# Optimization experiments

Hardware: AMD Instinct MI355X
Metric: run time of the kernel (lower is better)

Reference implementation:

```python
import jax, jax.numpy as jnp
import numpy as np
import math

EMB_DIM = 1024
NUM_HEADS = 16
D_H = EMB_DIM // NUM_HEADS
B, S = 2, 2048


def setup_inputs() -> dict:
    key = jax.random.key(0)
    ks = jax.random.split(key, 6)
    limit = math.sqrt(6.0 / (EMB_DIM + D_H))  # xavier_uniform per head
    x = jax.random.normal(ks[0], (B, S, EMB_DIM), dtype=jnp.float32)
    Wq = jax.random.uniform(ks[1], (NUM_HEADS, EMB_DIM, D_H), jnp.float32, -limit, limit)
    Wk = jax.random.uniform(ks[2], (NUM_HEADS, EMB_DIM, D_H), jnp.float32, -limit, limit)
    Wv = jax.random.uniform(ks[3], (NUM_HEADS, EMB_DIM, D_H), jnp.float32, -limit, limit)
    bq = jnp.zeros((NUM_HEADS, D_H), jnp.float32)
    bk = jnp.zeros((NUM_HEADS, D_H), jnp.float32)
    bv = jnp.zeros((NUM_HEADS, D_H), jnp.float32)
    limo = math.sqrt(6.0 / (EMB_DIM + EMB_DIM))
    W_O = jax.random.uniform(ks[4], (EMB_DIM, EMB_DIM), jnp.float32, -limo, limo)
    causal_mask = jnp.tril(jnp.ones((S, S), jnp.float32))
    padding_mask = jnp.zeros((B, S), jnp.bool_)  # all-False: nothing padded
    return {"x": x, "Wq": Wq, "bq": bq, "Wk": Wk, "bk": bk, "Wv": Wv,
            "bv": bv, "W_O": W_O, "causal_mask": causal_mask,
            "padding_mask": padding_mask}


def reference(x, Wq, bq, Wk, bk, Wv, bv, W_O, causal_mask, padding_mask):
    # Per-head projections, vectorized over heads: [B,S,E] x [H,E,D] -> [B,H,S,D]
    Q = jnp.einsum('bse,hed->bhsd', x, Wq) + bq[None, :, None, :]
    K = jnp.einsum('bse,hed->bhsd', x, Wk) + bk[None, :, None, :]
    V = jnp.einsum('bse,hed->bhsd', x, Wv) + bv[None, :, None, :]
    scores = jnp.einsum('bhsd,bhtd->bhst', Q, K) / math.sqrt(D_H)
    neg_inf = jnp.float32(-jnp.inf)
    scores = jnp.where(causal_mask[None, None, :, :] == 0, neg_inf, scores)
    scores = jnp.where(padding_mask[:, None, None, :], neg_inf, scores)
    attn = jax.nn.softmax(scores, axis=-1)
    out = jnp.einsum('bhst,bhtd->bhsd', attn, V)  # [B,H,S,D]
    # concat heads in order (dim=-1) -> [B,S,H*D]
    x_concat = out.transpose(0, 2, 1, 3).reshape(B, S, EMB_DIM)
    return x_concat @ W_O
```

## Files before the change

### kernel.cpp

```cpp
#include <hip/hip_runtime.h>
#include <hip/hip_bf16.h>


typedef __hip_bfloat16 bf16;
typedef __attribute__((ext_vector_type(8))) short bfrag;
typedef __attribute__((ext_vector_type(4))) float f32x4;
typedef __attribute__((ext_vector_type(16))) float f32x16;
typedef __attribute__((ext_vector_type(4))) short short4v;

#define MFMA16(a, b, c) __builtin_amdgcn_mfma_f32_16x16x32_bf16(a, b, c, 0, 0, 0)
#define MFMA32(a, b, c) __builtin_amdgcn_mfma_f32_32x32x16_bf16(a, b, c, 0, 0, 0)

__device__ __forceinline__ unsigned pkbf(float a, float b) {
  union { bf16 h[2]; unsigned u; } w;
  w.h[0] = __float2bfloat16(a);
  w.h[1] = __float2bfloat16(b);
  return w.u;
}

__global__ __launch_bounds__(256) void prep_all(const float* __restrict__ x,
                                                const float* __restrict__ Wq,
                                                const float* __restrict__ Wk,
                                                const float* __restrict__ Wv,
                                                const float* __restrict__ Wo,
                                                bf16* __restrict__ xb,
                                                bf16* __restrict__ WqkvT,
                                                bf16* __restrict__ WoT) {
  __shared__ bf16 tile[64][80];
  int id = blockIdx.x;
  int t = threadIdx.x;
  if (id < 2048) {
    int i = id * 2048 + t * 8;
    float4 a = *(const float4*)(x + i);
    float4 b = *(const float4*)(x + i + 4);
    union { bf16 h[8]; bfrag v; } tmp;
    tmp.h[0] = __float2bfloat16(a.x); tmp.h[1] = __float2bfloat16(a.y);
    tmp.h[2] = __float2bfloat16(a.z); tmp.h[3] = __float2bfloat16(a.w);
    tmp.h[4] = __float2bfloat16(b.x); tmp.h[5] = __float2bfloat16(b.y);
    tmp.h[6] = __float2bfloat16(b.z); tmp.h[7] = __float2bfloat16(b.w);
    *(bfrag*)(xb + i) = tmp.v;
    return;
  }
  int wid = id - 2048;
  const float* src;
  bf16* dst;
  int srcld, dstld, r0, c0;
  if (wid < 768) {
    int w = wid >> 8, h = (wid >> 4) & 15;
    r0 = (wid & 15) * 64; c0 = 0;
    src = ((w == 0) ? Wq : (w == 1) ? Wk : Wv) + (long)h * 1024 * 64;
    dst = WqkvT + ((long)w * 1024 + h * 64) * 1024;
    srcld = 64; dstld = 1024;
  } else {
    int j = wid - 768;
    c0 = (j & 15) * 64; r0 = (j >> 4) * 64;
    src = Wo; dst = WoT;
    srcld = 1024; dstld = 1024;
  }
  int lr = t >> 3, lc = (t & 7) << 3;
#pragma unroll
  for (int p = 0; p < 2; ++p) {
    int r = lr + p * 32;
    const float* s = src + (long)(r0 + r) * srcld + c0 + lc;
    union { bf16 h8[8]; bfrag v; } tmp;
#pragma unroll
    for (int j = 0; j < 8; ++j) tmp.h8[j] = __float2bfloat16(s[j]);
    *(bfrag*)(&tile[r][lc]) = tmp.v;
  }
  __syncthreads();
#pragma unroll
  for (int p = 0; p < 2; ++p) {
    int c = lr + p * 32;
    union { bf16 h8[8]; bfrag v; } tmp;
#pragma unroll
    for (int j = 0; j < 8; ++j) tmp.h8[j] = tile[lc + j][c];
    *(bfrag*)(dst + (long)(c0 + c) * dstld + r0 + lc) = tmp.v;
  }
}

__global__ __launch_bounds__(256) void gemm_qkv128(const bf16* __restrict__ xb,
                                                   const bf16* __restrict__ WT,
                                                   const float* __restrict__ bq,
                                                   const float* __restrict__ bk,
                                                   const float* __restrict__ bv,
                                                   bf16* __restrict__ Q,
                                                   bf16* __restrict__ K_,
                                                   bf16* __restrict__ Vt) {
  const int K = 1024;
  __shared__ bf16 As[128][72];
  __shared__ bf16 Bs[128][72];
  int id = blockIdx.x;
  int xcd = id & 7, sw = id >> 3;
  int m0 = ((xcd << 2) | (sw & 3)) * 128;
  int n0 = (sw >> 2) * 128;
  int t = threadIdx.x, wave = t >> 6, lane = t & 63, quad = lane >> 4, col = lane & 15;
  int wr = (wave >> 1) * 64, wc = (wave & 1) * 64;
  f32x4 acc[4][4] = {};

  int srow = t >> 1, scol = (t & 1) * 32;
  const bf16* Ag = xb + (long)(m0 + srow) * K + scol;
  const bf16* Bg = WT + (long)(n0 + srow) * K + scol;

  bfrag A0[4], B0[4], A1[4], B1[4];
#pragma unroll
  for (int i = 0; i < 4; ++i) {
    A0[i] = *(const bfrag*)(Ag + 8 * i);
    B0[i] = *(const bfrag*)(Bg + 8 * i);
    A1[i] = *(const bfrag*)(Ag + 64 + 8 * i);
    B1[i] = *(const bfrag*)(Bg + 64 + 8 * i);
  }

  for (int k0 = 0; k0 < K; k0 += 64) {
    __syncthreads();
#pragma unroll
    for (int i = 0; i < 4; ++i) {
      *(bfrag*)(&As[srow][scol + 8 * i]) = A0[i];
      *(bfrag*)(&Bs[srow][scol + 8 * i]) = B0[i];
    }
    int kn = (k0 + 128 < K) ? k0 + 128 : K - 64;
#pragma unroll
    for (int i = 0; i < 4; ++i) {
      A0[i] = A1[i]; B0[i] = B1[i];
      A1[i] = *(const bfrag*)(Ag + kn + 8 * i);
      B1[i] = *(const bfrag*)(Bg + kn + 8 * i);
    }
    __syncthreads();
#pragma unroll
    for (int kc = 0; kc < 2; ++kc) {
      bfrag ra[4], rb[4];
#pragma unroll
      for (int i = 0; i < 4; ++i)
        ra[i] = *(const bfrag*)(&As[wr + 16 * i + col][kc * 32 + quad * 8]);
#pragma unroll
      for (int c = 0; c < 4; ++c)
        rb[c] = *(const bfrag*)(&Bs[wc + 16 * c + col][kc * 32 + quad * 8]);
#pragma unroll
      for (int c = 0; c < 4; ++c)
#pragma unroll
        for (int i = 0; i < 4; ++i) acc[c][i] = MFMA16(ra[i], rb[c], acc[c][i]);
    }
  }

  int sel = n0 >> 10;
  const float* bias = (sel == 0) ? bq : (sel == 1) ? bk : bv;
#pragma unroll
  for (int c = 0; c < 4; ++c) {
    int nn = (n0 + wc + 16 * c + col) & 1023;
    float bvv = bias[nn];
    int h = nn >> 6, d = nn & 63;
#pragma unroll
    for (int i = 0; i < 4; ++i) {
      int mb = m0 + wr + 16 * i + quad * 4;
      int b = mb >> 11, s0 = mb & 2047;
      if (sel < 2) {
        bf16* dst = (sel == 0) ? Q : K_;
        long base = ((long)((b << 4) + h) * 2048 + s0) * 64 + d;
#pragma unroll
        for (int r = 0; r < 4; ++r)
          dst[base + (long)r * 64] = __float2bfloat16(acc[c][i][r] + bvv);
      } else {
        union { bf16 h4[4]; short4v v; } pk;
#pragma unroll
        for (int r = 0; r < 4; ++r) pk.h4[r] = __float2bfloat16(acc[c][i][r] + bvv);
        *(short4v*)(Vt + (long)(((b << 4) + h) * 64 + d) * 2048 + s0) = pk.v;
      }
    }
  }
}

__global__ __launch_bounds__(256) void gemm_out(const bf16* __restrict__ O,
                                                const bf16* __restrict__ Bt,
                                                float* __restrict__ Cf) {
  const int K = 1024;
  __shared__ bf16 As[128][72];
  __shared__ bf16 Bs[64][72];
  int id = blockIdx.x;
  int xcd = id & 7, sw = id >> 3;
  int m0 = ((xcd << 2) | (sw & 3)) * 128;
  int n0 = (sw >> 2) * 64;
  int t = threadIdx.x;
  int wave = t >> 6, lane = t & 63, quad = lane >> 4, col = lane & 15;
  int wr = (wave >> 1) * 64, wc = (wave & 1) * 32;
  f32x4 acc[2][4] = {};

  int srA = t >> 1, scA = (t & 1) * 32;
  int srB = t >> 2, scB = (t & 3) * 16;
  int mrow = m0 + srA;
  int ob = mrow >> 11, os = mrow & 2047;
  const bf16* Ag = O + (long)ob * 2097152 + (long)os * 64 + scA;
  const bf16* Bg = Bt + (long)(n0 + srB) * K + scB;

  bfrag A0[4], A1[4];
  bfrag B0[2], B1[2];
#pragma unroll
  for (int i = 0; i < 4; ++i) {
    A0[i] = *(const bfrag*)(Ag + 8 * i);
    A1[i] = *(const bfrag*)(Ag + (long)64 * 2048 + 8 * i);
  }
#pragma unroll
  for (int i = 0; i < 2; ++i) {
    B0[i] = *(const bfrag*)(Bg + 8 * i);
    B1[i] = *(const bfrag*)(Bg + 64 + 8 * i);
  }

  for (int k0 = 0; k0 < K; k0 += 64) {
    __syncthreads();
#pragma unroll
    for (int i = 0; i < 4; ++i) *(bfrag*)(&As[srA][scA + 8 * i]) = A0[i];
#pragma unroll
    for (int i = 0; i < 2; ++i) *(bfrag*)(&Bs[srB][scB + 8 * i]) = B0[i];
    int kn = (k0 + 128 < K) ? k0 + 128 : K - 64;
#pragma unroll
    for (int i = 0; i < 4; ++i) {
      A0[i] = A1[i];
      A1[i] = *(const bfrag*)(Ag + (long)kn * 2048 + 8 * i);
    }
#pragma unroll
    for (int i = 0; i < 2; ++i) {
      B0[i] = B1[i];
      B1[i] = *(const bfrag*)(Bg + kn + 8 * i);
    }
    __syncthreads();
#pragma unroll
    for (int kc = 0; kc < 2; ++kc) {
      bfrag ra[4], rb[2];
#pragma unroll
      for (int i = 0; i < 4; ++i)
        ra[i] = *(const bfrag*)(&As[wr + 16 * i + col][kc * 32 + quad * 8]);
#pragma unroll
      for (int c = 0; c < 2; ++c)
        rb[c] = *(const bfrag*)(&Bs[wc + 16 * c + col][kc * 32 + quad * 8]);
#pragma unroll
      for (int c = 0; c < 2; ++c)
#pragma unroll
        for (int i = 0; i < 4; ++i) acc[c][i] = MFMA16(ra[i], rb[c], acc[c][i]);
    }
  }

#pragma unroll
  for (int c = 0; c < 2; ++c) {
    int n = n0 + wc + 16 * c + col;
#pragma unroll
    for (int i = 0; i < 4; ++i)
#pragma unroll
      for (int r = 0; r < 4; ++r) {
        int m = m0 + wr + 16 * i + quad * 4 + r;
        Cf[(long)m * 1024 + n] = acc[c][i][r];
      }
  }
}

__global__ __launch_bounds__(256) void attn_kernel(const bf16* __restrict__ Q,
                                                   const bf16* __restrict__ K_,
                                                   const bf16* __restrict__ Vt,
                                                   bf16* __restrict__ O) {
  int id = blockIdx.x;
  int xcd = id & 7, jj = id >> 3;
  int qt = 31 - (jj >> 2);
  int bh = ((jj & 3) << 3) | xcd;

  __shared__ bf16 Ks[128][72];
  __shared__ bf16 Vs[64][136];

  int t = threadIdx.x, wave = t >> 6, lane = t & 63;
  int qh = wave >> 1, jh = wave & 1, hi = lane >> 5, l5 = lane & 31;

  const float SC2 = 0.18033688f;

  int krow = t >> 3, kg = (t & 7) * 8;
  int vrow = t >> 4, vg = (t & 15) * 8;
  const bf16* Kbase = K_ + ((long)bh * 2048 + krow) * 64 + kg;
  const bf16* Vbase = Vt + ((long)bh * 64 + vrow) * 2048 + vg;

  int q0 = qt * 64;
  int nj = (qt >> 1) + 1;
  int qi = q0 + 32 * qh + l5;

  bfrag qa[4];
  const bf16* qp = Q + ((long)bh * 2048 + q0 + 32 * qh + l5) * 64 + hi * 8;
#pragma unroll
  for (int kd = 0; kd < 4; ++kd) qa[kd] = *(const bfrag*)(qp + kd * 16);

  f32x16 o0, o1;
  float lsum = 0.f;
#pragma unroll
  for (int r = 0; r < 16; ++r) { o0[r] = 0.f; o1[r] = 0.f; }

  bfrag kreg[4], vreg[4];
#pragma unroll
  for (int i = 0; i < 4; ++i)
    kreg[i] = *(const bfrag*)(Kbase + (long)(32 * i) * 64);

  for (int jt = 0; jt < nj; ++jt) {
    int j0 = jt * 128;
    __syncthreads();
#pragma unroll
    for (int i = 0; i < 4; ++i)
      *(bfrag*)(&Ks[krow + 32 * i][kg]) = kreg[i];
    int jn = (jt + 1 < nj) ? (jt + 1) * 128 : jt * 128;
#pragma unroll
    for (int i = 0; i < 4; ++i)
      vreg[i] = *(const bfrag*)(Vbase + (long)(16 * i) * 2048 + j0);
#pragma unroll
    for (int i = 0; i < 4; ++i)
      kreg[i] = *(const bfrag*)(Kbase + (long)(jn + 32 * i) * 64);
    __syncthreads();

    f32x16 s0, s1;
#pragma unroll
    for (int r = 0; r < 16; ++r) { s0[r] = 0.f; s1[r] = 0.f; }
#pragma unroll
    for (int kd = 0; kd < 4; ++kd) {
      bfrag ka0 = *(const bfrag*)(&Ks[jh * 64 + l5][kd * 16 + hi * 8]);
      bfrag ka1 = *(const bfrag*)(&Ks[jh * 64 + 32 + l5][kd * 16 + hi * 8]);
      s0 = MFMA32(ka0, qa[kd], s0);
      s1 = MFMA32(ka1, qa[kd], s1);
    }

    bool lastT = (jt == nj - 1);
    unsigned g[2][4][2];
#pragma unroll
    for (int jb = 0; jb < 2; ++jb) {
      float pv[16];
#pragma unroll
      for (int r = 0; r < 16; ++r) {
        int jl = (r & 3) + 8 * (r >> 2) + 4 * hi;
        int j = j0 + jh * 64 + jb * 32 + jl;
        float sv = jb ? s1[r] : s0[r];
        float p = __builtin_amdgcn_exp2f(fmaf(sv, SC2, -16.0f));
        if (lastT) p = (j <= qi) ? p : 0.f;
        lsum += p;
        pv[r] = p;
      }
#pragma unroll
      for (int gg = 0; gg < 4; ++gg) {
        g[jb][gg][0] = pkbf(pv[4 * gg], pv[4 * gg + 1]);
        g[jb][gg][1] = pkbf(pv[4 * gg + 2], pv[4 * gg + 3]);
      }
    }
#pragma unroll
    for (int i = 0; i < 4; ++i)
      *(bfrag*)(&Vs[vrow + 16 * i][vg]) = vreg[i];
    __syncthreads();

#pragma unroll
    for (int jb = 0; jb < 2; ++jb) {
#pragma unroll
      for (int c = 0; c < 2; ++c) {
        unsigned a0 = g[jb][2 * c][0], a1 = g[jb][2 * c][1];
        unsigned b0 = g[jb][2 * c + 1][0], b1 = g[jb][2 * c + 1][1];
        unsigned sa0 = __shfl_xor((int)a0, 32, 64);
        unsigned sa1 = __shfl_xor((int)a1, 32, 64);
        unsigned sb0 = __shfl_xor((int)b0, 32, 64);
        unsigned sb1 = __shfl_xor((int)b1, 32, 64);
        union { unsigned u[4]; bfrag f; } pf;
        pf.u[0] = hi ? sb0 : a0;
        pf.u[1] = hi ? sb1 : a1;
        pf.u[2] = hi ? b0 : sa0;
        pf.u[3] = hi ? b1 : sa1;
        int kk = jh * 64 + jb * 32 + c * 16 + hi * 8;
        bfrag av0 = *(const bfrag*)(&Vs[l5][kk]);
        bfrag av1 = *(const bfrag*)(&Vs[32 + l5][kk]);
        o0 = MFMA32(av0, pf.f, o0);
        o1 = MFMA32(av1, pf.f, o1);
      }
    }
  }

  lsum += __shfl_xor(lsum, 32, 64);

  __syncthreads();
  float* Osc = (float*)&Ks[0][0];
  float* Lsc = (float*)&Vs[0][0];
  bf16* Of = (bf16*)((char*)&Vs[0][0] + 512);
  int q = 32 * qh + l5;
  if (jh == 1) {
#pragma unroll
    for (int r = 0; r < 16; ++r) {
      int d = (r & 3) + 8 * (r >> 2) + 4 * hi;
      Osc[q * 68 + d] = o0[r];
      Osc[q * 68 + 32 + d] = o1[r];
    }
    if (hi == 0) Lsc[q] = lsum;
  }
  __syncthreads();
  if (jh == 0) {
    float inv = 1.f / (lsum + Lsc[q]);
#pragma unroll
    for (int r = 0; r < 16; ++r) {
      int d = (r & 3) + 8 * (r >> 2) + 4 * hi;
      Of[q * 72 + d] = __float2bfloat16((o0[r] + Osc[q * 68 + d]) * inv);
      Of[q * 72 + 32 + d] = __float2bfloat16((o1[r] + Osc[q * 68 + 32 + d]) * inv);
    }
  }
  __syncthreads();
  int row = t >> 2, off = (t & 3) * 16;
  bf16* po = O + ((long)bh * 2048 + q0 + row) * 64 + off;
  *(bfrag*)(po) = *(const bfrag*)(&Of[row * 72 + off]);
  *(bfrag*)(po + 8) = *(const bfrag*)(&Of[row * 72 + off + 8]);
}

extern "C" void kernel_launch(void* const* d_in, const int* in_sizes, int n_in,
                              void* d_out, int out_size, void* d_ws, size_t ws_size,
                              hipStream_t stream) {
  const float* x  = (const float*)d_in[0];
  const float* Wq = (const float*)d_in[1];
  const float* bq = (const float*)d_in[2];
  const float* Wk = (const float*)d_in[3];
  const float* bk = (const float*)d_in[4];
  const float* Wv = (const float*)d_in[5];
  const float* bv = (const float*)d_in[6];
  const float* Wo = (const float*)d_in[7];
  float* out = (float*)d_out;

  bf16* ws = (bf16*)d_ws;
  const long MB1 = 1 << 20;
  bf16* WqkvT = ws + 0 * MB1;
  bf16* WoT   = ws + 3 * MB1;
  bf16* Q     = ws + 4 * MB1;
  bf16* K_    = ws + 8 * MB1;
  bf16* Vt    = ws + 12 * MB1;
  bf16* O     = ws + 16 * MB1;
  bf16* xb    = ws + 20 * MB1;

  prep_all<<<3072, 256, 0, stream>>>(x, Wq, Wk, Wv, Wo, xb, WqkvT, WoT);
  gemm_qkv128<<<768, 256, 0, stream>>>(xb, WqkvT, bq, bk, bv, Q, K_, Vt);
  attn_kernel<<<1024, 256, 0, stream>>>(Q, K_, Vt, O);
  gemm_out<<<512, 256, 0, stream>>>(O, WoT, out);
}
```

Before: 202.3 us.

## Fuse all MHA stages into one persistent kernel with grid barriers

Merges the four launches (conversion/transpose, QKV GEMM, attention, output GEMM) into a single persistent kernel of 768 blocks. Stages are separated by atomic-counter grid barriers, and attention tiles are handed out through an atomic work queue. The goal is to remove inter-kernel launch gaps and tail idle time, and to balance the uneven causal attention tiles. The counters live in the first bytes of the output buffer, which is zeroed by a memset. This relies on all 768 blocks being resident at once, enforced only through launch bounds, so it can deadlock if they are not. Spinning blocks may also still be polling a counter while the output GEMM starts overwriting that buffer with results.

```diff
diff --git a/kernel.cpp b/kernel.cpp
--- a/kernel.cpp
+++ b/kernel.cpp
@@ -18,386 +18,400 @@
   return w.u;
 }
 
-__global__ __launch_bounds__(256) void prep_all(const float* __restrict__ x,
-                                                const float* __restrict__ Wq,
-                                                const float* __restrict__ Wk,
-                                                const float* __restrict__ Wv,
-                                                const float* __restrict__ Wo,
-                                                bf16* __restrict__ xb,
-                                                bf16* __restrict__ WqkvT,
-                                                bf16* __restrict__ WoT) {
-  __shared__ bf16 tile[64][80];
-  int id = blockIdx.x;
-  int t = threadIdx.x;
-  if (id < 2048) {
-    int i = id * 2048 + t * 8;
-    float4 a = *(const float4*)(x + i);
-    float4 b = *(const float4*)(x + i + 4);
-    union { bf16 h[8]; bfrag v; } tmp;
-    tmp.h[0] = __float2bfloat16(a.x); tmp.h[1] = __float2bfloat16(a.y);
-    tmp.h[2] = __float2bfloat16(a.z); tmp.h[3] = __float2bfloat16(a.w);
-    tmp.h[4] = __float2bfloat16(b.x); tmp.h[5] = __float2bfloat16(b.y);
-    tmp.h[6] = __float2bfloat16(b.z); tmp.h[7] = __float2bfloat16(b.w);
-    *(bfrag*)(xb + i) = tmp.v;
-    return;
-  }
-  int wid = id - 2048;
-  const float* src;
-  bf16* dst;
-  int srcld, dstld, r0, c0;
-  if (wid < 768) {
-    int w = wid >> 8, h = (wid >> 4) & 15;
-    r0 = (wid & 15) * 64; c0 = 0;
-    src = ((w == 0) ? Wq : (w == 1) ? Wk : Wv) + (long)h * 1024 * 64;
-    dst = WqkvT + ((long)w * 1024 + h * 64) * 1024;
-    srcld = 64; dstld = 1024;
-  } else {
-    int j = wid - 768;
-    c0 = (j & 15) * 64; r0 = (j >> 4) * 64;
-    src = Wo; dst = WoT;
-    srcld = 1024; dstld = 1024;
-  }
-  int lr = t >> 3, lc = (t & 7) << 3;
-#pragma unroll
-  for (int p = 0; p < 2; ++p) {
-    int r = lr + p * 32;
-    const float* s = src + (long)(r0 + r) * srcld + c0 + lc;
-    union { bf16 h8[8]; bfrag v; } tmp;
-#pragma unroll
-    for (int j = 0; j < 8; ++j) tmp.h8[j] = __float2bfloat16(s[j]);
-    *(bfrag*)(&tile[r][lc]) = tmp.v;
+__device__ __forceinline__ void gbar(unsigned* c, unsigned target) {
+  __syncthreads();
+  if (threadIdx.x == 0) {
+    __threadfence();
+    __hip_atomic_fetch_add(c, 1u, __ATOMIC_RELEASE, __HIP_MEMORY_SCOPE_AGENT);
+    while (__hip_atomic_load(c, __ATOMIC_ACQUIRE, __HIP_MEMORY_SCOPE_AGENT) < target)
+      __builtin_amdgcn_s_sleep(32);
+    __threadfence();
   }
   __syncthreads();
-#pragma unroll
-  for (int p = 0; p < 2; ++p) {
-    int c = lr + p * 32;
-    union { bf16 h8[8]; bfrag v; } tmp;
-#pragma unroll
-    for (int j = 0; j < 8; ++j) tmp.h8[j] = tile[lc + j][c];
-    *(bfrag*)(dst + (long)(c0 + c) * dstld + r0 + lc) = tmp.v;
+}
+
+__global__ __launch_bounds__(256, 3) void mha_fused(
+    const float* __restrict__ x,
+    const float* __restrict__ Wq, const float* __restrict__ bq,
+    const float* __restrict__ Wk, const float* __restrict__ bk,
+    const float* __restrict__ Wv, const float* __restrict__ bv,
+    const float* __restrict__ Wo,
+    bf16* __restrict__ WqkvT, bf16* __restrict__ WoT,
+    bf16* __restrict__ Q, bf16* __restrict__ K_, bf16* __restrict__ Vt,
+    bf16* __restrict__ O, bf16* __restrict__ xb,
+    float* __restrict__ out, unsigned* cnt) {
+  __shared__ __align__(16) char SH[36880];
+  int id = blockIdx.x, t = threadIdx.x;
+
+  {
+    bf16(*tile)[80] = (bf16(*)[80])SH;
+    for (int item = id; item < 3072; item += 768) {
+      if (item < 1024) {
+        const float* src;
+        bf16* dst;
+        int srcld, dstld, r0, c0;
+        if (item < 768) {
+          int w = item >> 8, h = (item >> 4) & 15;
+          r0 = (item & 15) * 64; c0 = 0;
+          src = ((w == 0) ? Wq : (w == 1) ? Wk : Wv) + (long)h * 1024 * 64;
+          dst = WqkvT + ((long)w * 1024 + h * 64) * 1024;
+          srcld = 64; dstld = 1024;
+        } else {
+          int j = item - 768;
+          c0 = (j & 15) * 64; r0 = (j >> 4) * 64;
+          src = Wo; dst = WoT;
+          srcld = 1024; dstld = 1024;
+        }
+        int lr = t >> 3, lc = (t & 7) << 3;
+        __syncthreads();
+#pragma unroll
+        for (int p = 0; p < 2; ++p) {
+          int r = lr + p * 32;
+          const float* s = src + (long)(r0 + r) * srcld + c0 + lc;
+          union { bf16 h8[8]; bfrag v; } tmp;
+#pragma unroll
+          for (int j = 0; j < 8; ++j) tmp.h8[j] = __float2bfloat16(s[j]);
+          *(bfrag*)(&tile[r][lc]) = tmp.v;
+        }
+        __syncthreads();
+#pragma unroll
+        for (int p = 0; p < 2; ++p) {
+          int c = lr + p * 32;
+          union { bf16 h8[8]; bfrag v; } tmp;
+#pragma unroll
+          for (int j = 0; j < 8; ++j) tmp.h8[j] = tile[lc + j][c];
+          *(bfrag*)(dst + (long)(c0 + c) * dstld + r0 + lc) = tmp.v;
+        }
+      } else {
+        long i = (long)(item - 1024) * 2048 + t * 8;
+        float4 a = *(const float4*)(x + i);
+        float4 b = *(const float4*)(x + i + 4);
+        union { bf16 h[8]; bfrag v; } tmp;
+        tmp.h[0] = __float2bfloat16(a.x); tmp.h[1] = __float2bfloat16(a.y);
+        tmp.h[2] = __float2bfloat16(a.z); tmp.h[3] = __float2bfloat16(a.w);
+        tmp.h[4] = __float2bfloat16(b.x); tmp.h[5] = __float2bfloat16(b.y);
+        tmp.h[6] = __float2bfloat16(b.z); tmp.h[7] = __float2bfloat16(b.w);
+        *(bfrag*)(xb + i) = tmp.v;
+      }
+    }
   }
-}
-
-__global__ __launch_bounds__(256) void gemm_qkv128(const bf16* __restrict__ xb,
-                                                   const bf16* __restrict__ WT,
-                                                   const float* __restrict__ bq,
-                                                   const float* __restrict__ bk,
-                                                   const float* __restrict__ bv,
-                                                   bf16* __restrict__ Q,
-                                                   bf16* __restrict__ K_,
-                                                   bf16* __restrict__ Vt) {
-  const int K = 1024;
-  __shared__ bf16 As[128][72];
-  __shared__ bf16 Bs[128][72];
-  int id = blockIdx.x;
-  int xcd = id & 7, sw = id >> 3;
-  int m0 = ((xcd << 2) | (sw & 3)) * 128;
-  int n0 = (sw >> 2) * 128;
-  int t = threadIdx.x, wave = t >> 6, lane = t & 63, quad = lane >> 4, col = lane & 15;
-  int wr = (wave >> 1) * 64, wc = (wave & 1) * 64;
-  f32x4 acc[4][4] = {};
-
-  int srow = t >> 1, scol = (t & 1) * 32;
-  const bf16* Ag = xb + (long)(m0 + srow) * K + scol;
-  const bf16* Bg = WT + (long)(n0 + srow) * K + scol;
-
-  bfrag A0[4], B0[4], A1[4], B1[4];
-#pragma unroll
-  for (int i = 0; i < 4; ++i) {
-    A0[i] = *(const bfrag*)(Ag + 8 * i);
-    B0[i] = *(const bfrag*)(Bg + 8 * i);
-    A1[i] = *(const bfrag*)(Ag + 64 + 8 * i);
-    B1[i] = *(const bfrag*)(Bg + 64 + 8 * i);
+  gbar(cnt + 0, 768);
+
+  {
+    const int K = 1024;
+    bf16(*As)[72] = (bf16(*)[72])SH;
+    bf16(*Bs)[72] = (bf16(*)[72])(SH + 18432);
+    int xcd = id & 7, sw = id >> 3;
+    int m0 = ((xcd << 2) | (sw & 3)) * 128;
+    int n0 = (sw >> 2) * 128;
+    int wave = t >> 6, lane = t & 63, quad = lane >> 4, col = lane & 15;
+    int wr = (wave >> 1) * 64, wc = (wave & 1) * 64;
+    f32x4 acc[4][4] = {};
+
+    int srow = t >> 1, scol = (t & 1) * 32;
+    const bf16* Ag = xb + (long)(m0 + srow) * K + scol;
+    const bf16* Bg = WqkvT + (long)(n0 + srow) * K + scol;
+
+    bfrag A0[4], B0[4], A1[4], B1[4];
+#pragma unroll
+    for (int i = 0; i < 4; ++i) {
+      A0[i] = *(const bfrag*)(Ag + 8 * i);
+      B0[i] = *(const bfrag*)(Bg + 8 * i);
+      A1[i] = *(const bfrag*)(Ag + 64 + 8 * i);
+      B1[i] = *(const bfrag*)(Bg + 64 + 8 * i);
+    }
+
+    for (int k0 = 0; k0 < K; k0 += 64) {
+      __syncthreads();
+#pragma unroll
+      for (int i = 0; i < 4; ++i) {
+        *(bfrag*)(&As[srow][scol + 8 * i]) = A0[i];
+        *(bfrag*)(&Bs[srow][scol + 8 * i]) = B0[i];
+      }
+      int kn = (k0 + 128 < K) ? k0 + 128 : K - 64;
+#pragma unroll
+      for (int i = 0; i < 4; ++i) {
+        A0[i] = A1[i]; B0[i] = B1[i];
+        A1[i] = *(const bfrag*)(Ag + kn + 8 * i);
+        B1[i] = *(const bfrag*)(Bg + kn + 8 * i);
+      }
+      __syncthreads();
+#pragma unroll
+      for (int kc = 0; kc < 2; ++kc) {
+        bfrag ra[4], rb[4];
+#pragma unroll
+        for (int i = 0; i < 4; ++i)
+          ra[i] = *(const bfrag*)(&As[wr + 16 * i + col][kc * 32 + quad * 8]);
+#pragma unroll
+        for (int c = 0; c < 4; ++c)
+          rb[c] = *(const bfrag*)(&Bs[wc + 16 * c + col][kc * 32 + quad * 8]);
+#pragma unroll
+        for (int c = 0; c < 4; ++c)
+#pragma unroll
+          for (int i = 0; i < 4; ++i) acc[c][i] = MFMA16(ra[i], rb[c], acc[c][i]);
+      }
+    }
+
+    int sel = n0 >> 10;
+    const float* bias = (sel == 0) ? bq : (sel == 1) ? bk : bv;
+#pragma unroll
+    for (int c = 0; c < 4; ++c) {
+      int nn = (n0 + wc + 16 * c + col) & 1023;
+      float bvv = bias[nn];
+      int h = nn >> 6, d = nn & 63;
+#pragma unroll
+      for (int i = 0; i < 4; ++i) {
+        int mb = m0 + wr + 16 * i + quad * 4;
+        int b = mb >> 11, s0 = mb & 2047;
+        if (sel < 2) {
+          bf16* dst = (sel == 0) ? Q : K_;
+          long base = ((long)((b << 4) + h) * 2048 + s0) * 64 + d;
+#pragma unroll
+          for (int r = 0; r < 4; ++r)
+            dst[base + (long)r * 64] = __float2bfloat16(acc[c][i][r] + bvv);
+        } else {
+          union { bf16 h4[4]; short4v v; } pk;
+#pragma unroll
+          for (int r = 0; r < 4; ++r) pk.h4[r] = __float2bfloat16(acc[c][i][r] + bvv);
+          *(short4v*)(Vt + (long)(((b << 4) + h) * 64 + d) * 2048 + s0) = pk.v;
+        }
+      }
+    }
   }
-
-  for (int k0 = 0; k0 < K; k0 += 64) {
-    __syncthreads();
+  gbar(cnt + 1, 768);
+
+  {
+    bf16(*Ks)[72] = (bf16(*)[72])SH;
+    bf16(*Vs)[136] = (bf16(*)[136])(SH + 18432);
+    int* wslot = (int*)(SH + 36864);
+    int wave = t >> 6, lane = t & 63;
+    int qh = wave >> 1, jh = wave & 1, hi = lane >> 5, l5 = lane & 31;
+    const float SC2 = 0.18033688f;
+    int krow = t >> 3, kg = (t & 7) * 8;
+    int vrow = t >> 4, vg = (t & 15) * 8;
+
+    for (;;) {
+      __syncthreads();
+      if (t == 0)
+        *wslot = (int)__hip_atomic_fetch_add(cnt + 3, 1u, __ATOMIC_RELAXED,
+                                             __HIP_MEMORY_SCOPE_AGENT);
+      __syncthreads();
+      int item = *wslot;
+      if (item >= 1024) break;
+
+      int xcd = item & 7, jj = item >> 3;
+      int qt = 31 - (jj >> 2);
+      int bh = ((jj & 3) << 3) | xcd;
+
+      const bf16* Kbase = K_ + ((long)bh * 2048 + krow) * 64 + kg;
+      const bf16* Vbase = Vt + ((long)bh * 64 + vrow) * 2048 + vg;
+      int q0 = qt * 64;
+      int nj = (qt >> 1) + 1;
+      int qi = q0 + 32 * qh + l5;
+
+      bfrag qa[4];
+      const bf16* qp = Q + ((long)bh * 2048 + q0 + 32 * qh + l5) * 64 + hi * 8;
+#pragma unroll
+      for (int kd = 0; kd < 4; ++kd) qa[kd] = *(const bfrag*)(qp + kd * 16);
+
+      f32x16 o0, o1;
+      float lsum = 0.f;
+#pragma unroll
+      for (int r = 0; r < 16; ++r) { o0[r] = 0.f; o1[r] = 0.f; }
+
+      bfrag kreg[4], vreg[4];
+#pragma unroll
+      for (int i = 0; i < 4; ++i)
+        kreg[i] = *(const bfrag*)(Kbase + (long)(32 * i) * 64);
+
+      for (int jt = 0; jt < nj; ++jt) {
+        int j0 = jt * 128;
+        __syncthreads();
+#pragma unroll
+        for (int i = 0; i < 4; ++i)
+          *(bfrag*)(&Ks[krow + 32 * i][kg]) = kreg[i];
+        int jn = (jt + 1 < nj) ? (jt + 1) * 128 : jt * 128;
+#pragma unroll
+        for (int i = 0; i < 4; ++i)
+          vreg[i] = *(const bfrag*)(Vbase + (long)(16 * i) * 2048 + j0);
+#pragma unroll
+        for (int i = 0; i < 4; ++i)
+          kreg[i] = *(const bfrag*)(Kbase + (long)(jn + 32 * i) * 64);
+        __syncthreads();
+
+        f32x16 s0, s1;
+#pragma unroll
+        for (int r = 0; r < 16; ++r) { s0[r] = 0.f; s1[r] = 0.f; }
+#pragma unroll
+        for (int kd = 0; kd < 4; ++kd) {
+          bfrag ka0 = *(const bfrag*)(&Ks[jh * 64 + l5][kd * 16 + hi * 8]);
+          bfrag ka1 = *(const bfrag*)(&Ks[jh * 64 + 32 + l5][kd * 16 + hi * 8]);
+          s0 = MFMA32(ka0, qa[kd], s0);
+          s1 = MFMA32(ka1, qa[kd], s1);
+        }
+
+        bool lastT = (jt == nj - 1);
+        unsigned g[2][4][2];
+#pragma unroll
+        for (int jb = 0; jb < 2; ++jb) {
+          float pv[16];
+#pragma unroll
+          for (int r = 0; r < 16; ++r) {
+            int jl = (r & 3) + 8 * (r >> 2) + 4 * hi;
+            int j = j0 + jh * 64 + jb * 32 + jl;
+            float sv = jb ? s1[r] : s0[r];
+            float p = __builtin_amdgcn_exp2f(fmaf(sv, SC2, -16.0f));
+            if (lastT) p = (j <= qi) ? p : 0.f;
+            lsum += p;
+            pv[r] = p;
+          }
+#pragma unroll
+          for (int gg = 0; gg < 4; ++gg) {
+            g[jb][gg][0] = pkbf(pv[4 * gg], pv[4 * gg + 1]);
+            g[jb][gg][1] = pkbf(pv[4 * gg + 2], pv[4 * gg + 3]);
+          }
+        }
+#pragma unroll
+        for (int i = 0; i < 4; ++i)
+          *(bfrag*)(&Vs[vrow + 16 * i][vg]) = vreg[i];
+        __syncthreads();
+
+#pragma unroll
+        for (int jb = 0; jb < 2; ++jb) {
+#pragma unroll
+          for (int c = 0; c < 2; ++c) {
+            unsigned a0 = g[jb][2 * c][0], a1 = g[jb][2 * c][1];
+            unsigned b0 = g[jb][2 * c + 1][0], b1 = g[jb][2 * c + 1][1];
+            unsigned sa0 = __shfl_xor((int)a0, 32, 64);
+            unsigned sa1 = __shfl_xor((int)a1, 32, 64);
+            unsigned sb0 = __shfl_xor((int)b0, 32, 64);
+            unsigned sb1 = __shfl_xor((int)b1, 32, 64);
+            union { unsigned u[4]; bfrag f; } pf;
+            pf.u[0] = hi ? sb0 : a0;
+            pf.u[1] = hi ? sb1 : a1;
+            pf.u[2] = hi ? b0 : sa0;
+            pf.u[3] = hi ? b1 : sa1;
+            int kk = jh * 64 + jb * 32 + c * 16 + hi * 8;
+            bfrag av0 = *(const bfrag*)(&Vs[l5][kk]);
+            bfrag av1 = *(const bfrag*)(&Vs[32 + l5][kk]);
+            o0 = MFMA32(av0, pf.f, o0);
+            o1 = MFMA32(av1, pf.f, o1);
+          }
+        }
+      }
+
+      lsum += __shfl_xor(lsum, 32, 64);
+
+      __syncthreads();
+      float* Osc = (float*)&Ks[0][0];
+      float* Lsc = (float*)&Vs[0][0];
+      bf16* Of = (bf16*)((char*)&Vs[0][0] + 512);
+      int q = 32 * qh + l5;
+      if (jh == 1) {
+#pragma unroll
+        for (int r = 0; r < 16; ++r) {
+          int d = (r & 3) + 8 * (r >> 2) + 4 * hi;
+          Osc[q * 68 + d] = o0[r];
+          Osc[q * 68 + 32 + d] = o1[r];
+        }
+        if (hi == 0) Lsc[q] = lsum;
+      }
+      __syncthreads();
+      if (jh == 0) {
+        float inv = 1.f / (lsum + Lsc[q]);
+#pragma unroll
+        for (int r = 0; r < 16; ++r) {
+          int d = (r & 3) + 8 * (r >> 2) + 4 * hi;
+          Of[q * 72 + d] = __float2bfloat16((o0[r] + Osc[q * 68 + d]) * inv);
+          Of[q * 72 + 32 + d] = __float2bfloat16((o1[r] + Osc[q * 68 + 32 + d]) * inv);
+        }
+      }
+      __syncthreads();
+      int row = t >> 2, off = (t & 3) * 16;
+      bf16* po = O + ((long)bh * 2048 + q0 + row) * 64 + off;
+      *(bfrag*)(po) = *(const bfrag*)(&Of[row * 72 + off]);
+      *(bfrag*)(po + 8) = *(const bfrag*)(&Of[row * 72 + off + 8]);
+    }
+  }
+  gbar(cnt + 2, 768);
+
+  if (id < 512) {
+    const int K = 1024;
+    bf16(*As)[72] = (bf16(*)[72])SH;
+    bf16(*Bs)[72] = (bf16(*)[72])(SH + 18432);
+    int xcd = id & 7, sw = id >> 3;
+    int m0 = ((xcd << 2) | (sw & 3)) * 128;
+    int n0 = (sw >> 2) * 64;
+    int wave = t >> 6, lane = t & 63, quad = lane >> 4, col = lane & 15;
+    int wr = (wave >> 1) * 64, wc = (wave & 1) * 32;
+    f32x4 acc[2][4] = {};
+
+    int srA = t >> 1, scA = (t & 1) * 32;
+    int srB = t >> 2, scB = (t & 3) * 16;
+    int mrow = m0 + srA;
+    int ob = mrow >> 11, os = mrow & 2047;
+    const bf16* Ag = O + (long)ob * 2097152 + (long)os * 64 + scA;
+    const bf16* Bg = WoT + (long)(n0 + srB) * K + scB;
+
+    bfrag A0[4], A1[4];
+    bfrag B0[2], B1[2];
 #pragma unroll
     for (int i = 0; i < 4; ++i) {
-      *(bfrag*)(&As[srow][scol + 8 * i]) = A0[i];
-      *(bfrag*)(&Bs[srow][scol + 8 * i]) = B0[i];
-    }
-    int kn = (k0 + 128 < K) ? k0 + 128 : K - 64;
-#pragma unroll
-    for (int i = 0; i < 4; ++i) {
-      A0[i] = A1[i]; B0[i] = B1[i];
-      A1[i] = *(const bfrag*)(Ag + kn + 8 * i);
-      B1[i] = *(const bfrag*)(Bg + kn + 8 * i);
-    }
-    __syncthreads();
-#pragma unroll
-    for (int kc = 0; kc < 2; ++kc) {
-      bfrag ra[4], rb[4];
+      A0[i] = *(const bfrag*)(Ag + 8 * i);
+      A1[i] = *(const bfrag*)(Ag + (long)64 * 2048 + 8 * i);
+    }
+#pragma unroll
+    for (int i = 0; i < 2; ++i) {
+      B0[i] = *(const bfrag*)(Bg + 8 * i);
+      B1[i] = *(const bfrag*)(Bg + 64 + 8 * i);
+    }
+
+    for (int k0 = 0; k0 < K; k0 += 64) {
+      __syncthreads();
+#pragma unroll
+      for (int i = 0; i < 4; ++i) *(bfrag*)(&As[srA][scA + 8 * i]) = A0[i];
+#pragma unroll
+      for (int i = 0; i < 2; ++i) *(bfrag*)(&Bs[srB][scB + 8 * i]) = B0[i];
+      int kn = (k0 + 128 < K) ? k0 + 128 : K - 64;
+#pragma unroll
+      for (int i = 0; i < 4; ++i) {
+        A0[i] = A1[i];
+        A1[i] = *(const bfrag*)(Ag + (long)kn * 2048 + 8 * i);
+      }
+#pragma unroll
+      for (int i = 0; i < 2; ++i) {
+        B0[i] = B1[i];
+        B1[i] = *(const bfrag*)(Bg + kn + 8 * i);
+      }
+      __syncthreads();
+#pragma unroll
+      for (int kc = 0; kc < 2; ++kc) {
+        bfrag ra[4], rb[2];
+#pragma unroll
+        for (int i = 0; i < 4; ++i)
+          ra[i] = *(const bfrag*)(&As[wr + 16 * i + col][kc * 32 + quad * 8]);
+#pragma unroll
+        for (int c = 0; c < 2; ++c)
+          rb[c] = *(const bfrag*)(&Bs[wc + 16 * c + col][kc * 32 + quad * 8]);
+#pragma unroll
+        for (int c = 0; c < 2; ++c)
+#pragma unroll
+          for (int i = 0; i < 4; ++i) acc[c][i] = MFMA16(ra[i], rb[c], acc[c][i]);
+      }
+    }
+
+#pragma unroll
+    for (int c = 0; c < 2; ++c) {
+      int n = n0 + wc + 16 * c + col;
 #pragma unroll
       for (int i = 0; i < 4; ++i)
-        ra[i] = *(const bfrag*)(&As[wr + 16 * i + col][kc * 32 + quad * 8]);
-#pragma unroll
-      for (int c = 0; c < 4; ++c)
-        rb[c] = *(const bfrag*)(&Bs[wc + 16 * c + col][kc * 32 + quad * 8]);
-#pragma unroll
-      for (int c = 0; c < 4; ++c)
-#pragma unroll
-        for (int i = 0; i < 4; ++i) acc[c][i] = MFMA16(ra[i], rb[c], acc[c][i]);
+#pragma unroll
+        for (int r = 0; r < 4; ++r) {
+          int m = m0 + wr + 16 * i + quad * 4 + r;
+          out[(long)m * 1024 + n] = acc[c][i][r];
+        }
     }
   }
-
-  int sel = n0 >> 10;
-  const float* bias = (sel == 0) ? bq : (sel == 1) ? bk : bv;
-#pragma unroll
-  for (int c = 0; c < 4; ++c) {
-    int nn = (n0 + wc + 16 * c + col) & 1023;
-    float bvv = bias[nn];
-    int h = nn >> 6, d = nn & 63;
-#pragma unroll
-    for (int i = 0; i < 4; ++i) {
-      int mb = m0 + wr + 16 * i + quad * 4;
-      int b = mb >> 11, s0 = mb & 2047;
-      if (sel < 2) {
-        bf16* dst = (sel == 0) ? Q : K_;
-        long base = ((long)((b << 4) + h) * 2048 + s0) * 64 + d;
-#pragma unroll
-        for (int r = 0; r < 4; ++r)
-          dst[base + (long)r * 64] = __float2bfloat16(acc[c][i][r] + bvv);
-      } else {
-        union { bf16 h4[4]; short4v v; } pk;
-#pragma unroll
-        for (int r = 0; r < 4; ++r) pk.h4[r] = __float2bfloat16(acc[c][i][r] + bvv);
-        *(short4v*)(Vt + (long)(((b << 4) + h) * 64 + d) * 2048 + s0) = pk.v;
-      }
-    }
-  }
-}
-
-__global__ __launch_bounds__(256) void gemm_out(const bf16* __restrict__ O,
-                                                const bf16* __restrict__ Bt,
-                                                float* __restrict__ Cf) {
-  const int K = 1024;
-  __shared__ bf16 As[128][72];
-  __shared__ bf16 Bs[64][72];
-  int id = blockIdx.x;
-  int xcd = id & 7, sw = id >> 3;
-  int m0 = ((xcd << 2) | (sw & 3)) * 128;
-  int n0 = (sw >> 2) * 64;
-  int t = threadIdx.x;
-  int wave = t >> 6, lane = t & 63, quad = lane >> 4, col = lane & 15;
-  int wr = (wave >> 1) * 64, wc = (wave & 1) * 32;
-  f32x4 acc[2][4] = {};
-
-  int srA = t >> 1, scA = (t & 1) * 32;
-  int srB = t >> 2, scB = (t & 3) * 16;
-  int mrow = m0 + srA;
-  int ob = mrow >> 11, os = mrow & 2047;
-  const bf16* Ag = O + (long)ob * 2097152 + (long)os * 64 + scA;
-  const bf16* Bg = Bt + (long)(n0 + srB) * K + scB;
-
-  bfrag A0[4], A1[4];
-  bfrag B0[2], B1[2];
-#pragma unroll
-  for (int i = 0; i < 4; ++i) {
-    A0[i] = *(const bfrag*)(Ag + 8 * i);
-    A1[i] = *(const bfrag*)(Ag + (long)64 * 2048 + 8 * i);
-  }
-#pragma unroll
-  for (int i = 0; i < 2; ++i) {
-    B0[i] = *(const bfrag*)(Bg + 8 * i);
-    B1[i] = *(const bfrag*)(Bg + 64 + 8 * i);
-  }
-
-  for (int k0 = 0; k0 < K; k0 += 64) {
-    __syncthreads();
-#pragma unroll
-    for (int i = 0; i < 4; ++i) *(bfrag*)(&As[srA][scA + 8 * i]) = A0[i];
-#pragma unroll
-    for (int i = 0; i < 2; ++i) *(bfrag*)(&Bs[srB][scB + 8 * i]) = B0[i];
-    int kn = (k0 + 128 < K) ? k0 + 128 : K - 64;
-#pragma unroll
-    for (int i = 0; i < 4; ++i) {
-      A0[i] = A1[i];
-      A1[i] = *(const bfrag*)(Ag + (long)kn * 2048 + 8 * i);
-    }
-#pragma unroll
-    for (int i = 0; i < 2; ++i) {
-      B0[i] = B1[i];
-      B1[i] = *(const bfrag*)(Bg + kn + 8 * i);
-    }
-    __syncthreads();
-#pragma unroll
-    for (int kc = 0; kc < 2; ++kc) {
-      bfrag ra[4], rb[2];
-#pragma unroll
-      for (int i = 0; i < 4; ++i)
-        ra[i] = *(const bfrag*)(&As[wr + 16 * i + col][kc * 32 + quad * 8]);
-#pragma unroll
-      for (int c = 0; c < 2; ++c)
-        rb[c] = *(const bfrag*)(&Bs[wc + 16 * c + col][kc * 32 + quad * 8]);
-#pragma unroll
-      for (int c = 0; c < 2; ++c)
-#pragma unroll
-        for (int i = 0; i < 4; ++i) acc[c][i] = MFMA16(ra[i], rb[c], acc[c][i]);
-    }
-  }
-
-#pragma unroll
-  for (int c = 0; c < 2; ++c) {
-    int n = n0 + wc + 16 * c + col;
-#pragma unroll
-    for (int i = 0; i < 4; ++i)
-#pragma unroll
-      for (int r = 0; r < 4; ++r) {
-        int m = m0 + wr + 16 * i + quad * 4 + r;
-        Cf[(long)m * 1024 + n] = acc[c][i][r];
-      }
-  }
-}
-
-__global__ __launch_bounds__(256) void attn_kernel(const bf16* __restrict__ Q,
-                                                   const bf16* __restrict__ K_,
-                                                   const bf16* __restrict__ Vt,
-                                                   bf16* __restrict__ O) {
-  int id = blockIdx.x;
-  int xcd = id & 7, jj = id >> 3;
-  int qt = 31 - (jj >> 2);
-  int bh = ((jj & 3) << 3) | xcd;
-
-  __shared__ bf16 Ks[128][72];
-  __shared__ bf16 Vs[64][136];
-
-  int t = threadIdx.x, wave = t >> 6, lane = t & 63;
-  int qh = wave >> 1, jh = wave & 1, hi = lane >> 5, l5 = lane & 31;
-
-  const float SC2 = 0.18033688f;
-
-  int krow = t >> 3, kg = (t & 7) * 8;
-  int vrow = t >> 4, vg = (t & 15) * 8;
-  const bf16* Kbase = K_ + ((long)bh * 2048 + krow) * 64 + kg;
-  const bf16* Vbase = Vt + ((long)bh * 64 + vrow) * 2048 + vg;
-
-  int q0 = qt * 64;
-  int nj = (qt >> 1) + 1;
-  int qi = q0 + 32 * qh + l5;
-
-  bfrag qa[4];
-  const bf16* qp = Q + ((long)bh * 2048 + q0 + 32 * qh + l5) * 64 + hi * 8;
-#pragma unroll
-  for (int kd = 0; kd < 4; ++kd) qa[kd] = *(const bfrag*)(qp + kd * 16);
-
-  f32x16 o0, o1;
-  float lsum = 0.f;
-#pragma unroll
-  for (int r = 0; r < 16; ++r) { o0[r] = 0.f; o1[r] = 0.f; }
-
-  bfrag kreg[4], vreg[4];
-#pragma unroll
-  for (int i = 0; i < 4; ++i)
-    kreg[i] = *(const bfrag*)(Kbase + (long)(32 * i) * 64);
-
-  for (int jt = 0; jt < nj; ++jt) {
-    int j0 = jt * 128;
-    __syncthreads();
-#pragma unroll
-    for (int i = 0; i < 4; ++i)
-      *(bfrag*)(&Ks[krow + 32 * i][kg]) = kreg[i];
-    int jn = (jt + 1 < nj) ? (jt + 1) * 128 : jt * 128;
-#pragma unroll
-    for (int i = 0; i < 4; ++i)
-      vreg[i] = *(const bfrag*)(Vbase + (long)(16 * i) * 2048 + j0);
-#pragma unroll
-    for (int i = 0; i < 4; ++i)
-      kreg[i] = *(const bfrag*)(Kbase + (long)(jn + 32 * i) * 64);
-    __syncthreads();
-
-    f32x16 s0, s1;
-#pragma unroll
-    for (int r = 0; r < 16; ++r) { s0[r] = 0.f; s1[r] = 0.f; }
-#pragma unroll
-    for (int kd = 0; kd < 4; ++kd) {
-      bfrag ka0 = *(const bfrag*)(&Ks[jh * 64 + l5][kd * 16 + hi * 8]);
-      bfrag ka1 = *(const bfrag*)(&Ks[jh * 64 + 32 + l5][kd * 16 + hi * 8]);
-      s0 = MFMA32(ka0, qa[kd], s0);
-      s1 = MFMA32(ka1, qa[kd], s1);
-    }
-
-    bool lastT = (jt == nj - 1);
-    unsigned g[2][4][2];
-#pragma unroll
-    for (int jb = 0; jb < 2; ++jb) {
-      float pv[16];
-#pragma unroll
-      for (int r = 0; r < 16; ++r) {
-        int jl = (r & 3) + 8 * (r >> 2) + 4 * hi;
-        int j = j0 + jh * 64 + jb * 32 + jl;
-        float sv = jb ? s1[r] : s0[r];
-        float p = __builtin_amdgcn_exp2f(fmaf(sv, SC2, -16.0f));
-        if (lastT) p = (j <= qi) ? p : 0.f;
-        lsum += p;
-        pv[r] = p;
-      }
-#pragma unroll
-      for (int gg = 0; gg < 4; ++gg) {
-        g[jb][gg][0] = pkbf(pv[4 * gg], pv[4 * gg + 1]);
-        g[jb][gg][1] = pkbf(pv[4 * gg + 2], pv[4 * gg + 3]);
-      }
-    }
-#pragma unroll
-    for (int i = 0; i < 4; ++i)
-      *(bfrag*)(&Vs[vrow + 16 * i][vg]) = vreg[i];
-    __syncthreads();
-
-#pragma unroll
-    for (int jb = 0; jb < 2; ++jb) {
-#pragma unroll
-      for (int c = 0; c < 2; ++c) {
-        unsigned a0 = g[jb][2 * c][0], a1 = g[jb][2 * c][1];
-        unsigned b0 = g[jb][2 * c + 1][0], b1 = g[jb][2 * c + 1][1];
-        unsigned sa0 = __shfl_xor((int)a0, 32, 64);
-        unsigned sa1 = __shfl_xor((int)a1, 32, 64);
-        unsigned sb0 = __shfl_xor((int)b0, 32, 64);
-        unsigned sb1 = __shfl_xor((int)b1, 32, 64);
-        union { unsigned u[4]; bfrag f; } pf;
-        pf.u[0] = hi ? sb0 : a0;
-        pf.u[1] = hi ? sb1 : a1;
-        pf.u[2] = hi ? b0 : sa0;
-        pf.u[3] = hi ? b1 : sa1;
-        int kk = jh * 64 + jb * 32 + c * 16 + hi * 8;
-        bfrag av0 = *(const bfrag*)(&Vs[l5][kk]);
-        bfrag av1 = *(const bfrag*)(&Vs[32 + l5][kk]);
-        o0 = MFMA32(av0, pf.f, o0);
-        o1 = MFMA32(av1, pf.f, o1);
-      }
-    }
-  }
-
-  lsum += __shfl_xor(lsum, 32, 64);
-
-  __syncthreads();
-  float* Osc = (float*)&Ks[0][0];
-  float* Lsc = (float*)&Vs[0][0];
-  bf16* Of = (bf16*)((char*)&Vs[0][0] + 512);
-  int q = 32 * qh + l5;
-  if (jh == 1) {
-#pragma unroll
-    for (int r = 0; r < 16; ++r) {
-      int d = (r & 3) + 8 * (r >> 2) + 4 * hi;
-      Osc[q * 68 + d] = o0[r];
-      Osc[q * 68 + 32 + d] = o1[r];
-    }
-    if (hi == 0) Lsc[q] = lsum;
-  }
-  __syncthreads();
-  if (jh == 0) {
-    float inv = 1.f / (lsum + Lsc[q]);
-#pragma unroll
-    for (int r = 0; r < 16; ++r) {
-      int d = (r & 3) + 8 * (r >> 2) + 4 * hi;
-      Of[q * 72 + d] = __float2bfloat16((o0[r] + Osc[q * 68 + d]) * inv);
-      Of[q * 72 + 32 + d] = __float2bfloat16((o1[r] + Osc[q * 68 + 32 + d]) * inv);
-    }
-  }
-  __syncthreads();
-  int row = t >> 2, off = (t & 3) * 16;
-  bf16* po = O + ((long)bh * 2048 + q0 + row) * 64 + off;
-  *(bfrag*)(po) = *(const bfrag*)(&Of[row * 72 + off]);
-  *(bfrag*)(po + 8) = *(const bfrag*)(&Of[row * 72 + off + 8]);
 }
 
 extern "C" void kernel_launch(void* const* d_in, const int* in_sizes, int n_in,
@@ -423,8 +437,8 @@
   bf16* O     = ws + 16 * MB1;
   bf16* xb    = ws + 20 * MB1;
 
-  prep_all<<<3072, 256, 0, stream>>>(x, Wq, Wk, Wv, Wo, xb, WqkvT, WoT);
-  gemm_qkv128<<<768, 256, 0, stream>>>(xb, WqkvT, bq, bk, bv, Q, K_, Vt);
-  attn_kernel<<<1024, 256, 0, stream>>>(Q, K_, Vt, O);
-  gemm_out<<<512, 256, 0, stream>>>(O, WoT, out);
+  hipMemsetAsync(d_out, 0, 64, stream);
+  mha_fused<<<768, 256, 0, stream>>>(x, Wq, bq, Wk, bk, Wv, bv, Wo,
+                                     WqkvT, WoT, Q, K_, Vt, O, xb,
+                                     out, (unsigned*)d_out);
 }
```

Measured after the change: 671.9 us. 232% more time.
